# Kernel optimization log

Measured on AMD Instinct MI355X. Metric: run time of the kernel, lower is better.

The kernel has to match this reference:

```python
import jax, jax.numpy as jnp
import numpy as np

# Stack of L SSA transformer blocks (SMVDR conv_trans stages with sr_ratio=2)
L, B, N, C = 4, 64, 196, 768          # layers, batch(=16 samples x 4 views), tokens, dim
CN = 960                               # c_new = int(C * 1.25)
HID = 3072                             # mlp hidden = 4*C
NH = 12                                # heads
HD, HDK = C // NH, CN // NH            # v head dim 64, q/k head dim 80
SR, HW = 2, 14                         # spatial reduction ratio, sqrt(N)


def _ln(x, g, b, eps):
    m = jnp.mean(x, axis=-1, keepdims=True)
    v = jnp.var(x, axis=-1, keepdims=True)
    return (x - m) * jax.lax.rsqrt(v + eps) * g + b


def setup_inputs() -> dict:
    key = jax.random.key(0)
    ks = jax.random.split(key, 12)
    s = jnp.float32(0.02)

    def rn(k, shape):
        return jax.random.normal(k, shape, jnp.float32) * s

    return {
        "x": jax.random.normal(ks[0], (B, N, C), jnp.float32),
        "q_w": rn(ks[1], (L, C, CN)),                 # q projection (no bias)
        "dw_w": rn(ks[2], (L, C, 1, SR, SR)),         # depthwise reduction conv (OIHW, groups=C)
        "dw_b": jnp.zeros((L, C), jnp.float32),
        "pw_w": rn(ks[3], (L, C, CN)),                # 1x1 conv C -> c_new
        "pw_b": jnp.zeros((L, CN), jnp.float32),
        "lnr_g": jnp.ones((L, CN), jnp.float32),      # norm_act LayerNorm (eps 1e-5)
        "lnr_b": jnp.zeros((L, CN), jnp.float32),
        "k_w": rn(ks[4], (L, CN, CN)),
        "v_w": rn(ks[5], (L, CN, C)),
        "proj_w": rn(ks[6], (L, C, C)),
        "proj_b": jnp.zeros((L, C), jnp.float32),
        "ln1_g": jnp.ones((L, C), jnp.float32),
        "ln1_b": jnp.zeros((L, C), jnp.float32),
        "ln2_g": jnp.ones((L, C), jnp.float32),
        "ln2_b": jnp.zeros((L, C), jnp.float32),
        "fc1_w": rn(ks[7], (L, C, HID)),
        "fc1_b": jnp.zeros((L, HID), jnp.float32),
        "fc2_w": rn(ks[8], (L, HID, C)),
        "fc2_b": jnp.zeros((L, C), jnp.float32),
    }


def reference(x, q_w, dw_w, dw_b, pw_w, pw_b, lnr_g, lnr_b, k_w, v_w,
              proj_w, proj_b, ln1_g, ln1_b, ln2_g, ln2_b,
              fc1_w, fc1_b, fc2_w, fc2_b):
    scale = 1.0 / jnp.sqrt(jnp.float32(HD) * 1.25)   # (head_dim * c_ratio) ** -0.5
    for l in range(L):
        # --- SSA attention branch ---
        y = _ln(x, ln1_g[l], ln1_b[l], 1e-6)
        img = y.transpose(0, 2, 1).reshape(B, C, HW, HW)
        # strided depthwise conv reduction (kernel=stride=sr_ratio, groups=C)
        r = jax.lax.conv_general_dilated(
            img, dw_w[l], window_strides=(SR, SR), padding='VALID',
            feature_group_count=C,
            dimension_numbers=('NCHW', 'OIHW', 'NCHW'))
        r = r + dw_b[l][None, :, None, None]
        r = jnp.einsum('bchw,cd->bhwd', r, pw_w[l]) + pw_b[l]   # 1x1 conv -> (B,7,7,CN)
        r = r.reshape(B, -1, CN)                                 # (B, M=49, CN)
        r = jax.nn.gelu(_ln(r, lnr_g[l], lnr_b[l], 1e-5), approximate=False)
        q = (y @ q_w[l]).reshape(B, N, NH, HDK).transpose(0, 2, 1, 3)   # (B,H,N,80)
        k = (r @ k_w[l]).reshape(B, -1, NH, HDK).transpose(0, 2, 1, 3)  # (B,H,M,80)
        v = (r @ v_w[l]).reshape(B, -1, NH, HD).transpose(0, 2, 1, 3)   # (B,H,M,64)
        attn = jax.nn.softmax(jnp.einsum('bhnd,bhmd->bhnm', q, k) * scale, axis=-1)
        o = jnp.einsum('bhnm,bhmd->bnhd', attn, v).reshape(B, N, C)
        x = x + o @ proj_w[l] + proj_b[l]
        # --- MLP branch ---
        z = _ln(x, ln2_g[l], ln2_b[l], 1e-6)
        h = jax.nn.gelu(z @ fc1_w[l] + fc1_b[l], approximate=False)
        x = x + h @ fc2_w[l] + fc2_b[l]
    return x
```

## Files before the change

### kernel.cpp

```cpp
#include <hip/hip_runtime.h>
#include <hip/hip_bf16.h>
#include <math.h>

#define L_LAYERS 4
#define BSZ 64
#define NTOK 196
#define CDIM 768
#define CNDIM 960
#define HIDDIM 3072
#define NHEAD 12
#define HD 64
#define HDK 80
#define MRED 49
#define ROWS (BSZ*NTOK)
#define RROWS (BSZ*MRED)
#define KVN 1728

typedef __bf16 bf16x8 __attribute__((ext_vector_type(8)));
typedef float f32x4 __attribute__((ext_vector_type(4)));
typedef unsigned short u16x4 __attribute__((ext_vector_type(4)));

static __device__ inline float bf2f(unsigned short u) {
    unsigned int x = ((unsigned int)u) << 16;
    return __builtin_bit_cast(float, x);
}
static __device__ inline unsigned short f2bf(float f) {
    return __builtin_bit_cast(unsigned short, __float2bfloat16(f));
}
static __device__ inline unsigned int pack2bf(float lo, float hi) {
    return (unsigned int)f2bf(lo) | ((unsigned int)f2bf(hi) << 16);
}
static __device__ inline float gelu_f(float x) {
    float t = x * (1.5957691216f + 0.0713548162f * x * x);
    return x * __builtin_amdgcn_rcpf(1.0f + __expf(-t));
}

#define GLLDS16(gsrc, ldst)                                                        \
    __builtin_amdgcn_global_load_lds(                                              \
        (const __attribute__((address_space(1))) unsigned int*)(const void*)(gsrc),\
        (__attribute__((address_space(3))) unsigned int*)(void*)(ldst), 16, 0, 0)

__global__ void transpose_bf16_kernel(const float* __restrict__ src,
                                      unsigned short* __restrict__ dst,
                                      int K, int N, size_t srcLS, size_t dstLS) {
    __shared__ float tile[32][33];
    const float* s = src + (size_t)blockIdx.z * srcLS;
    unsigned short* d = dst + (size_t)blockIdx.z * dstLS;
    int k0 = blockIdx.y * 32, n0 = blockIdx.x * 32;
#pragma unroll
    for (int i = 0; i < 4; i++) {
        int k = k0 + threadIdx.y + i * 8, n = n0 + threadIdx.x;
        if (k < K && n < N) tile[threadIdx.y + i * 8][threadIdx.x] = s[(size_t)k * N + n];
    }
    __syncthreads();
#pragma unroll
    for (int i = 0; i < 4; i++) {
        int n = n0 + threadIdx.y + i * 8, k = k0 + threadIdx.x;
        if (n < N && k < K) d[(size_t)n * K + k] = f2bf(tile[threadIdx.x][threadIdx.y + i * 8]);
    }
}

__global__ void ln_kernel(const float* __restrict__ x, const float* __restrict__ g,
                          const float* __restrict__ b, unsigned short* __restrict__ y,
                          int M, int C, float eps, int do_gelu) {
    int row = blockIdx.x * 4 + (threadIdx.x >> 6);
    int lane = threadIdx.x & 63;
    if (row >= M) return;
    const float* xr = x + (size_t)row * C;
    float s = 0.f, ss = 0.f;
    for (int c = lane; c < C; c += 64) { float v = xr[c]; s += v; ss += v * v; }
#pragma unroll
    for (int off = 32; off; off >>= 1) { s += __shfl_down(s, off); ss += __shfl_down(ss, off); }
    s = __shfl(s, 0); ss = __shfl(ss, 0);
    float mean = s / (float)C;
    float var = ss / (float)C - mean * mean;
    float rstd = rsqrtf(var + eps);
    unsigned short* yr = y + (size_t)row * C;
    for (int c = lane; c < C; c += 64) {
        float v = (xr[c] - mean) * rstd * g[c] + b[c];
        if (do_gelu) v = gelu_f(v);
        yr[c] = f2bf(v);
    }
}

__global__ void dwconv_kernel(const unsigned short* __restrict__ y,
                              const float* __restrict__ w,
                              const float* __restrict__ bias,
                              unsigned short* __restrict__ r0) {
    int bm = blockIdx.x;
    int b = bm / MRED, m = bm % MRED;
    int i = m / 7, j = m % 7;
    int r00 = b * NTOK + (2 * i) * 14 + 2 * j;
    for (int c = threadIdx.x; c < CDIM; c += 256) {
        float acc = bias[c];
        acc += bf2f(y[(size_t)(r00)      * CDIM + c]) * w[c * 4 + 0];
        acc += bf2f(y[(size_t)(r00 + 1)  * CDIM + c]) * w[c * 4 + 1];
        acc += bf2f(y[(size_t)(r00 + 14) * CDIM + c]) * w[c * 4 + 2];
        acc += bf2f(y[(size_t)(r00 + 15) * CDIM + c]) * w[c * 4 + 3];
        r0[(size_t)bm * CDIM + c] = f2bf(acc);
    }
}

template <int MODE>
__global__ __launch_bounds__(512, 2) void gemm256_kernel(
    const unsigned short* __restrict__ A,
    const unsigned short* __restrict__ Bt,
    const float* __restrict__ bias,
    float* __restrict__ outF,
    unsigned short* __restrict__ outB,
    int M, int N, int K, int NR, int NC) {
    extern __shared__ __align__(16) char sb[];

    int id = blockIdx.x;
    int gsize = 8 * NC;
    int g = id / gsize;
    int local = id - g * gsize;
    int rbase = g * 8;
    int Gg = NR - rbase; if (Gg > 8) Gg = 8;
    int col = local / Gg;
    int row = rbase + (local - col * Gg);
    int m0 = row * 256, n0 = col * 256;

    int tid = threadIdx.x;
    int w = tid >> 6, lane = tid & 63, quad = lane >> 4, l16 = lane & 15;
    int wm = w >> 2, wn = w & 3;

    int sr = tid >> 2;
    int qs = ((tid & 3) - ((sr >> 1) & 3)) & 3;
    const unsigned short* aS0 = A  + (size_t)(m0 + sr) * K + qs * 8;
    const unsigned short* aS1 = A  + (size_t)(m0 + sr + 128) * K + qs * 8;
    const unsigned short* bS0 = Bt + (size_t)(n0 + sr) * K + qs * 8;
    const unsigned short* bS1 = Bt + (size_t)(n0 + sr + 128) * K + qs * 8;

    int sq16 = ((quad + (l16 >> 1)) & 3) * 16;
    int aOff = (wm * 128 + l16) * 64 + sq16;
    int bOff = 16384 + (wn * 64 + l16) * 64 + sq16;

    f32x4 zero4 = {0.f, 0.f, 0.f, 0.f};
    f32x4 acc[8][4];
#pragma unroll
    for (int mi = 0; mi < 8; mi++)
#pragma unroll
        for (int ni = 0; ni < 4; ni++) acc[mi][ni] = zero4;

    int NT = K >> 5;

#define STAGE256(slotptr, koff)                                  \
    do {                                                         \
        GLLDS16(aS0 + (koff), (slotptr) + w * 1024);             \
        GLLDS16(aS1 + (koff), (slotptr) + 8192  + w * 1024);     \
        GLLDS16(bS0 + (koff), (slotptr) + 16384 + w * 1024);     \
        GLLDS16(bS1 + (koff), (slotptr) + 24576 + w * 1024);     \
    } while (0)

    STAGE256(sb, 0);
    STAGE256(sb + 32768, 32);
    asm volatile("s_waitcnt vmcnt(4)" ::: "memory");
    __builtin_amdgcn_s_barrier();

    for (int t = 0; t < NT; ++t) {
        char* sc = sb + (size_t)(t & 3) * 32768;
        if (t + 2 < NT) {
            char* sp = sb + (size_t)((t + 2) & 3) * 32768;
            STAGE256(sp, (t + 2) * 32);
        }
        bf16x8 bfr[4], af[4];
#pragma unroll
        for (int ni = 0; ni < 4; ni++)
            bfr[ni] = *(const bf16x8*)(sc + bOff + ni * 1024);
#pragma unroll
        for (int mi = 0; mi < 4; mi++)
            af[mi] = *(const bf16x8*)(sc + aOff + mi * 1024);
        __builtin_amdgcn_s_setprio(1);
#pragma unroll
        for (int mi = 0; mi < 4; mi++)
#pragma unroll
            for (int ni = 0; ni < 4; ni++)
                acc[mi][ni] = __builtin_amdgcn_mfma_f32_16x16x32_bf16(
                    af[mi], bfr[ni], acc[mi][ni], 0, 0, 0);
        __builtin_amdgcn_s_setprio(0);
#pragma unroll
        for (int mi = 0; mi < 4; mi++)
            af[mi] = *(const bf16x8*)(sc + aOff + (mi + 4) * 1024);
        __builtin_amdgcn_s_setprio(1);
#pragma unroll
        for (int mi = 0; mi < 4; mi++)
#pragma unroll
            for (int ni = 0; ni < 4; ni++)
                acc[mi + 4][ni] = __builtin_amdgcn_mfma_f32_16x16x32_bf16(
                    af[mi], bfr[ni], acc[mi + 4][ni], 0, 0, 0);
        __builtin_amdgcn_s_setprio(0);
        if (t + 2 < NT) {
            asm volatile("s_waitcnt vmcnt(4)" ::: "memory");
        } else {
            asm volatile("s_waitcnt vmcnt(0)" ::: "memory");
        }
        __builtin_amdgcn_s_barrier();
    }
#undef STAGE256

    __syncthreads();
    float* eld = (float*)(sb + w * 16384);
    int colbase = n0 + wn * 64;
#pragma unroll
    for (int mi = 0; mi < 8; mi++) {
#pragma unroll
        for (int ni = 0; ni < 4; ni++)
#pragma unroll
            for (int rr = 0; rr < 4; rr++)
                eld[(quad * 4 + rr) * 64 + ni * 16 + l16] = acc[mi][ni][rr];
        int rowb = m0 + wm * 128 + mi * 16;
#pragma unroll
        for (int p = 0; p < 4; p++) {
            int r = p * 4 + quad;
            int c = l16 * 4;
            int gr = rowb + r, gc = colbase + c;
            if (gr < M && gc < N) {
                f32x4 v4 = *(f32x4*)(eld + r * 64 + c);
                if (MODE == 0) {
                    u16x4 h;
#pragma unroll
                    for (int e = 0; e < 4; e++) h[e] = f2bf(v4[e]);
                    *(u16x4*)(outB + (size_t)gr * N + gc) = h;
                } else {
                    f32x4 b4 = *(const f32x4*)(bias + gc);
                    if (MODE == 1) {
                        *(f32x4*)(outF + (size_t)gr * N + gc) = v4 + b4;
                    } else if (MODE == 2) {
                        f32x4 o4 = *(f32x4*)(outF + (size_t)gr * N + gc);
                        *(f32x4*)(outF + (size_t)gr * N + gc) = o4 + v4 + b4;
                    } else {
                        u16x4 h;
#pragma unroll
                        for (int e = 0; e < 4; e++) h[e] = f2bf(gelu_f(v4[e] + b4[e]));
                        *(u16x4*)(outB + (size_t)gr * N + gc) = h;
                    }
                }
            }
        }
    }
}

__global__ __launch_bounds__(512, 4) void attn_kernel(
    const unsigned short* __restrict__ qb,
    const unsigned short* __restrict__ kv,
    unsigned short* __restrict__ ob) {
    __shared__ __align__(16) unsigned short Ks[64 * 96];
    __shared__ __align__(16) unsigned short V2[64 * 136];
    __shared__ __align__(16) unsigned short Os[8 * 16 * 72];

    int bh = blockIdx.x;
    int b = bh / NHEAD, h = bh % NHEAD;
    int tid = threadIdx.x;

    for (int idx = tid; idx < 49 * 8; idx += 512) {
        int m = idx >> 3, c = idx & 7;
        ((unsigned int*)Ks)[m * 48 + 40 + c] = 0u;
    }
    for (int idx = tid; idx < 49 * 10; idx += 512) {
        int m = idx / 10, c = idx % 10;
        bf16x8 v = *(const bf16x8*)(kv + (size_t)(b * MRED + m) * KVN + h * HDK + c * 8);
        *(bf16x8*)(Ks + m * 96 + c * 8) = v;
    }
    for (int idx = tid; idx < 64 * 128; idx += 512) {
        int d = idx >> 7, c = idx & 127;
        int s = c >> 5, q = (c >> 3) & 3, j = c & 7;
        int kt = s * 32 + ((j >> 2) << 4) + q * 4 + (j & 3);
        unsigned short val = 0;
        if (kt < MRED) val = kv[(size_t)(b * MRED + kt) * KVN + 960 + h * HD + d];
        V2[d * 136 + c] = val;
    }
    __syncthreads();

    int wv = tid >> 6, lane = tid & 63, quad = lane >> 4, l16 = lane & 15;
    unsigned short* Ow = Os + wv * 16 * 72;
    const float scale = 0.11180339887498949f;
    f32x4 zero4 = {0.f, 0.f, 0.f, 0.f};

#pragma unroll
    for (int gi = 0; gi < 2; ++gi) {
        int qg = wv + gi * 8;
        if (qg >= 13) break;
        const unsigned short* qrow =
            qb + (size_t)(b * NTOK + qg * 16 + l16) * CNDIM + h * HDK + quad * 8;
        bf16x8 bq0 = *(const bf16x8*)(qrow);
        bf16x8 bq1 = *(const bf16x8*)(qrow + 32);
        bf16x8 bq2 = *(const bf16x8*)(qrow + 64);

        f32x4 sf[4];
#pragma unroll
        for (int kf = 0; kf < 4; kf++) sf[kf] = zero4;
#pragma unroll
        for (int kf = 0; kf < 4; kf++) {
            const unsigned short* kr = Ks + (kf * 16 + l16) * 96 + quad * 8;
            sf[kf] = __builtin_amdgcn_mfma_f32_16x16x32_bf16(
                *(const bf16x8*)(kr), bq0, sf[kf], 0, 0, 0);
            sf[kf] = __builtin_amdgcn_mfma_f32_16x16x32_bf16(
                *(const bf16x8*)(kr + 32), bq1, sf[kf], 0, 0, 0);
            sf[kf] = __builtin_amdgcn_mfma_f32_16x16x32_bf16(
                *(const bf16x8*)(kr + 64), bq2, sf[kf], 0, 0, 0);
        }

        float p[4][4];
        float mx = -1e30f;
#pragma unroll
        for (int kf = 0; kf < 4; kf++)
#pragma unroll
            for (int r = 0; r < 4; r++) {
                float v = sf[kf][r] * scale;
                if (kf == 3) {
                    v = (r == 0 && quad == 0) ? v : -1e30f;
                }
                p[kf][r] = v;
                mx = fmaxf(mx, v);
            }
        mx = fmaxf(mx, __shfl_xor(mx, 16));
        mx = fmaxf(mx, __shfl_xor(mx, 32));
        float sum = 0.f;
#pragma unroll
        for (int kf = 0; kf < 4; kf++)
#pragma unroll
            for (int r = 0; r < 4; r++) {
                float e = __expf(p[kf][r] - mx);
                p[kf][r] = e;
                sum += e;
            }
        sum += __shfl_xor(sum, 16);
        sum += __shfl_xor(sum, 32);
        float inv = 1.0f / sum;
#pragma unroll
        for (int kf = 0; kf < 4; kf++)
#pragma unroll
            for (int r = 0; r < 4; r++) p[kf][r] *= inv;

        unsigned int W[4][2];
#pragma unroll
        for (int kf = 0; kf < 4; kf++) {
            W[kf][0] = pack2bf(p[kf][0], p[kf][1]);
            W[kf][1] = pack2bf(p[kf][2], p[kf][3]);
        }

        f32x4 oacc[4];
#pragma unroll
        for (int df = 0; df < 4; df++) oacc[df] = zero4;
#pragma unroll
        for (int s = 0; s < 2; s++) {
            union { unsigned int u[4]; bf16x8 v; } bb;
            bb.u[0] = W[2 * s][0];
            bb.u[1] = W[2 * s][1];
            bb.u[2] = W[2 * s + 1][0];
            bb.u[3] = W[2 * s + 1][1];
#pragma unroll
            for (int df = 0; df < 4; df++) {
                const unsigned short* vr = V2 + (df * 16 + l16) * 136 + s * 32 + quad * 8;
                oacc[df] = __builtin_amdgcn_mfma_f32_16x16x32_bf16(
                    *(const bf16x8*)(vr), bb.v, oacc[df], 0, 0, 0);
            }
        }

#pragma unroll
        for (int df = 0; df < 4; df++) {
#pragma unroll
            for (int wp = 0; wp < 2; wp++) {
                unsigned int pk = pack2bf(oacc[df][2 * wp], oacc[df][2 * wp + 1]);
                *(unsigned int*)(Ow + l16 * 72 + df * 16 + quad * 4 + 2 * wp) = pk;
            }
        }
        int q = lane >> 2, cch = lane & 3;
        int grow = qg * 16 + q;
        if (grow < NTOK) {
            unsigned short* dst = ob + (size_t)(b * NTOK + grow) * CDIM + h * HD + cch * 8;
            bf16x8 v0 = *(const bf16x8*)(Ow + q * 72 + cch * 8);
            bf16x8 v1 = *(const bf16x8*)(Ow + q * 72 + cch * 8 + 32);
            *(bf16x8*)(dst) = v0;
            *(bf16x8*)(dst + 32) = v1;
        }
    }
}


extern "C" void kernel_launch(void* const* d_in, const int* in_sizes, int n_in,
                              void* d_out, int out_size, void* d_ws, size_t ws_size,
                              hipStream_t stream) {
    (void)in_sizes; (void)n_in; (void)out_size; (void)ws_size;
    const float* x_in   = (const float*)d_in[0];
    const float* q_w    = (const float*)d_in[1];
    const float* dw_w   = (const float*)d_in[2];
    const float* dw_b   = (const float*)d_in[3];
    const float* pw_w   = (const float*)d_in[4];
    const float* pw_b   = (const float*)d_in[5];
    const float* lnr_g  = (const float*)d_in[6];
    const float* lnr_b  = (const float*)d_in[7];
    const float* k_w    = (const float*)d_in[8];
    const float* v_w    = (const float*)d_in[9];
    const float* proj_w = (const float*)d_in[10];
    const float* proj_b = (const float*)d_in[11];
    const float* ln1_g  = (const float*)d_in[12];
    const float* ln1_b  = (const float*)d_in[13];
    const float* ln2_g  = (const float*)d_in[14];
    const float* ln2_b  = (const float*)d_in[15];
    const float* fc1_w  = (const float*)d_in[16];
    const float* fc1_b  = (const float*)d_in[17];
    const float* fc2_w  = (const float*)d_in[18];
    const float* fc2_b  = (const float*)d_in[19];
    float* xout = (float*)d_out;
    char* ws = (char*)d_ws;

    static bool attr_done = false;
    if (!attr_done) {
        hipFuncSetAttribute(reinterpret_cast<const void*>(&gemm256_kernel<0>),
                            hipFuncAttributeMaxDynamicSharedMemorySize, 131072);
        hipFuncSetAttribute(reinterpret_cast<const void*>(&gemm256_kernel<1>),
                            hipFuncAttributeMaxDynamicSharedMemorySize, 131072);
        hipFuncSetAttribute(reinterpret_cast<const void*>(&gemm256_kernel<2>),
                            hipFuncAttributeMaxDynamicSharedMemorySize, 131072);
        hipFuncSetAttribute(reinterpret_cast<const void*>(&gemm256_kernel<3>),
                            hipFuncAttributeMaxDynamicSharedMemorySize, 131072);
        attr_done = true;
    }

    const size_t PL = 8601600;
    const size_t offQ = 0, offPW = 786432, offKV = 1572864,
                 offPJ = 3293184, offF1 = 3883008, offF2 = 6242304;
    unsigned short* W = (unsigned short*)ws;
    char* act = ws + PL * 2 * L_LAYERS;
    unsigned short* y_bf = (unsigned short*)act;
    char* blk = act + (size_t)ROWS * CDIM * 2;
    unsigned short* q_bf  = (unsigned short*)(blk);
    unsigned short* r0_bf = (unsigned short*)(blk + 24084480);
    float*          pw_f  = (float*)        (blk + 29196288);
    unsigned short* r_bf  = (unsigned short*)(blk + 41238528);
    unsigned short* kv_bf = (unsigned short*)(blk + 47628288);
    unsigned short* o_bf  = (unsigned short*)(blk + 58466304);
    unsigned short* h_bf  = (unsigned short*)(blk);
    unsigned short* z_bf  = y_bf;

    hipMemcpyAsync(xout, x_in, (size_t)ROWS * CDIM * sizeof(float),
                   hipMemcpyDeviceToDevice, stream);

    dim3 tb(32, 8);
    transpose_bf16_kernel<<<dim3(CNDIM / 32, CDIM / 32, L_LAYERS), tb, 0, stream>>>(
        q_w, W + offQ, CDIM, CNDIM, (size_t)CDIM * CNDIM, PL);
    transpose_bf16_kernel<<<dim3(CNDIM / 32, CDIM / 32, L_LAYERS), tb, 0, stream>>>(
        pw_w, W + offPW, CDIM, CNDIM, (size_t)CDIM * CNDIM, PL);
    transpose_bf16_kernel<<<dim3(CNDIM / 32, CNDIM / 32, L_LAYERS), tb, 0, stream>>>(
        k_w, W + offKV, CNDIM, CNDIM, (size_t)CNDIM * CNDIM, PL);
    transpose_bf16_kernel<<<dim3(CDIM / 32, CNDIM / 32, L_LAYERS), tb, 0, stream>>>(
        v_w, W + offKV + (size_t)CNDIM * CNDIM, CNDIM, CDIM, (size_t)CNDIM * CDIM, PL);
    transpose_bf16_kernel<<<dim3(CDIM / 32, CDIM / 32, L_LAYERS), tb, 0, stream>>>(
        proj_w, W + offPJ, CDIM, CDIM, (size_t)CDIM * CDIM, PL);
    transpose_bf16_kernel<<<dim3(HIDDIM / 32, CDIM / 32, L_LAYERS), tb, 0, stream>>>(
        fc1_w, W + offF1, CDIM, HIDDIM, (size_t)CDIM * HIDDIM, PL);
    transpose_bf16_kernel<<<dim3(CDIM / 32, HIDDIM / 32, L_LAYERS), tb, 0, stream>>>(
        fc2_w, W + offF2, HIDDIM, CDIM, (size_t)HIDDIM * CDIM, PL);

    for (int l = 0; l < L_LAYERS; l++) {
        const unsigned short* wl = W + (size_t)l * PL;
        ln_kernel<<<ROWS / 4, 256, 0, stream>>>(xout, ln1_g + l * CDIM, ln1_b + l * CDIM,
                                                y_bf, ROWS, CDIM, 1e-6f, 0);
        gemm256_kernel<0><<<49 * 4, 512, 131072, stream>>>(
            y_bf, wl + offQ, nullptr, nullptr, q_bf, ROWS, CNDIM, CDIM, 49, 4);
        dwconv_kernel<<<RROWS, 256, 0, stream>>>(y_bf, dw_w + (size_t)l * CDIM * 4,
                                                 dw_b + l * CDIM, r0_bf);
        gemm256_kernel<1><<<13 * 4, 512, 131072, stream>>>(
            r0_bf, wl + offPW, pw_b + l * CNDIM, pw_f, nullptr, RROWS, CNDIM, CDIM, 13, 4);
        ln_kernel<<<RROWS / 4, 256, 0, stream>>>(pw_f, lnr_g + l * CNDIM, lnr_b + l * CNDIM,
                                                 r_bf, RROWS, CNDIM, 1e-5f, 1);
        gemm256_kernel<0><<<13 * 7, 512, 131072, stream>>>(
            r_bf, wl + offKV, nullptr, nullptr, kv_bf, RROWS, KVN, CNDIM, 13, 7);
        attn_kernel<<<BSZ * NHEAD, 512, 0, stream>>>(q_bf, kv_bf, o_bf);
        gemm256_kernel<2><<<49 * 3, 512, 131072, stream>>>(
            o_bf, wl + offPJ, proj_b + l * CDIM, xout, nullptr, ROWS, CDIM, CDIM, 49, 3);
        ln_kernel<<<ROWS / 4, 256, 0, stream>>>(xout, ln2_g + l * CDIM, ln2_b + l * CDIM,
                                                z_bf, ROWS, CDIM, 1e-6f, 0);
        gemm256_kernel<3><<<49 * 12, 512, 131072, stream>>>(
            z_bf, wl + offF1, fc1_b + l * HIDDIM, nullptr, h_bf, ROWS, HIDDIM, CDIM, 49, 12);
        gemm256_kernel<2><<<49 * 3, 512, 131072, stream>>>(
            h_bf, wl + offF2, fc2_b + l * CDIM, xout, nullptr, ROWS, CDIM, HIDDIM, 49, 3);
    }
}
```

Baseline: 1.813 ms.

## Replace 256x256 GEMM tiles with 128-row tiles and double-buffered LDS

The GEMM kernel drops from 256x256 tiles with a 4-slot, 2-ahead prefetch pipeline to 128xBN tiles (BN 256 or 128) with a 2-slot double buffer. Shared memory per block falls from 128KB to 32-48KB, and launch bounds ask for 4 blocks per CU. The goal is more blocks and better wave fill on the small M=3136 reduced-row GEMMs and the large GEMMs. In exchange, each tile reuses less data, the pipeline is shallower with a full vmcnt(0) wait every iteration, and global traffic for weights and activations rises.

```diff
diff --git a/kernel.cpp b/kernel.cpp
--- a/kernel.cpp
+++ b/kernel.cpp
@@ -101,14 +101,16 @@
     }
 }
 
-template <int MODE>
-__global__ __launch_bounds__(512, 2) void gemm256_kernel(
+template <int MODE, int BN>
+__global__ __launch_bounds__(512, 4) void gemm128_kernel(
     const unsigned short* __restrict__ A,
     const unsigned short* __restrict__ Bt,
     const float* __restrict__ bias,
     float* __restrict__ outF,
     unsigned short* __restrict__ outB,
     int M, int N, int K, int NR, int NC) {
+    constexpr int NFR = BN / 64;
+    constexpr int SLOT = 8192 + BN * 64;
     extern __shared__ __align__(16) char sb[];
 
     int id = blockIdx.x;
@@ -119,7 +121,7 @@
     int Gg = NR - rbase; if (Gg > 8) Gg = 8;
     int col = local / Gg;
     int row = rbase + (local - col * Gg);
-    int m0 = row * 256, n0 = col * 256;
+    int m0 = row * 128, n0 = col * BN;
 
     int tid = threadIdx.x;
     int w = tid >> 6, lane = tid & 63, quad = lane >> 4, l16 = lane & 15;
@@ -128,95 +130,78 @@
     int sr = tid >> 2;
     int qs = ((tid & 3) - ((sr >> 1) & 3)) & 3;
     const unsigned short* aS0 = A  + (size_t)(m0 + sr) * K + qs * 8;
-    const unsigned short* aS1 = A  + (size_t)(m0 + sr + 128) * K + qs * 8;
     const unsigned short* bS0 = Bt + (size_t)(n0 + sr) * K + qs * 8;
     const unsigned short* bS1 = Bt + (size_t)(n0 + sr + 128) * K + qs * 8;
 
     int sq16 = ((quad + (l16 >> 1)) & 3) * 16;
-    int aOff = (wm * 128 + l16) * 64 + sq16;
-    int bOff = 16384 + (wn * 64 + l16) * 64 + sq16;
+    int aOff = (wm * 64 + l16) * 64 + sq16;
+    int bOff = 8192 + (wn * (BN / 4) + l16) * 64 + sq16;
 
     f32x4 zero4 = {0.f, 0.f, 0.f, 0.f};
-    f32x4 acc[8][4];
-#pragma unroll
-    for (int mi = 0; mi < 8; mi++)
-#pragma unroll
-        for (int ni = 0; ni < 4; ni++) acc[mi][ni] = zero4;
+    f32x4 acc[4][NFR];
+#pragma unroll
+    for (int mi = 0; mi < 4; mi++)
+#pragma unroll
+        for (int ni = 0; ni < NFR; ni++) acc[mi][ni] = zero4;
 
     int NT = K >> 5;
 
-#define STAGE256(slotptr, koff)                                  \
-    do {                                                         \
-        GLLDS16(aS0 + (koff), (slotptr) + w * 1024);             \
-        GLLDS16(aS1 + (koff), (slotptr) + 8192  + w * 1024);     \
-        GLLDS16(bS0 + (koff), (slotptr) + 16384 + w * 1024);     \
-        GLLDS16(bS1 + (koff), (slotptr) + 24576 + w * 1024);     \
-    } while (0)
-
-    STAGE256(sb, 0);
-    STAGE256(sb + 32768, 32);
-    asm volatile("s_waitcnt vmcnt(4)" ::: "memory");
+    {
+        GLLDS16(aS0, sb + w * 1024);
+        GLLDS16(bS0, sb + 8192 + w * 1024);
+        if constexpr (BN == 256) GLLDS16(bS1, sb + 16384 + w * 1024);
+    }
+    asm volatile("s_waitcnt vmcnt(0)" ::: "memory");
     __builtin_amdgcn_s_barrier();
 
     for (int t = 0; t < NT; ++t) {
-        char* sc = sb + (size_t)(t & 3) * 32768;
-        if (t + 2 < NT) {
-            char* sp = sb + (size_t)((t + 2) & 3) * 32768;
-            STAGE256(sp, (t + 2) * 32);
-        }
-        bf16x8 bfr[4], af[4];
-#pragma unroll
-        for (int ni = 0; ni < 4; ni++)
-            bfr[ni] = *(const bf16x8*)(sc + bOff + ni * 1024);
+        char* sc = sb + (size_t)(t & 1) * SLOT;
+        if (t + 1 < NT) {
+            char* sp = sb + (size_t)((t + 1) & 1) * SLOT;
+            int koff = (t + 1) * 32;
+            GLLDS16(aS0 + koff, sp + w * 1024);
+            GLLDS16(bS0 + koff, sp + 8192 + w * 1024);
+            if constexpr (BN == 256) GLLDS16(bS1 + koff, sp + 16384 + w * 1024);
+        }
+        bf16x8 af[4], bfr[NFR];
 #pragma unroll
         for (int mi = 0; mi < 4; mi++)
             af[mi] = *(const bf16x8*)(sc + aOff + mi * 1024);
+#pragma unroll
+        for (int ni = 0; ni < NFR; ni++)
+            bfr[ni] = *(const bf16x8*)(sc + bOff + ni * 1024);
         __builtin_amdgcn_s_setprio(1);
 #pragma unroll
         for (int mi = 0; mi < 4; mi++)
 #pragma unroll
-            for (int ni = 0; ni < 4; ni++)
+            for (int ni = 0; ni < NFR; ni++)
                 acc[mi][ni] = __builtin_amdgcn_mfma_f32_16x16x32_bf16(
                     af[mi], bfr[ni], acc[mi][ni], 0, 0, 0);
         __builtin_amdgcn_s_setprio(0);
-#pragma unroll
-        for (int mi = 0; mi < 4; mi++)
-            af[mi] = *(const bf16x8*)(sc + aOff + (mi + 4) * 1024);
-        __builtin_amdgcn_s_setprio(1);
-#pragma unroll
-        for (int mi = 0; mi < 4; mi++)
-#pragma unroll
-            for (int ni = 0; ni < 4; ni++)
-                acc[mi + 4][ni] = __builtin_amdgcn_mfma_f32_16x16x32_bf16(
-                    af[mi], bfr[ni], acc[mi + 4][ni], 0, 0, 0);
-        __builtin_amdgcn_s_setprio(0);
-        if (t + 2 < NT) {
-            asm volatile("s_waitcnt vmcnt(4)" ::: "memory");
-        } else {
-            asm volatile("s_waitcnt vmcnt(0)" ::: "memory");
-        }
+        asm volatile("s_waitcnt vmcnt(0)" ::: "memory");
         __builtin_amdgcn_s_barrier();
     }
-#undef STAGE256
 
     __syncthreads();
-    float* eld = (float*)(sb + w * 16384);
-    int colbase = n0 + wn * 64;
-#pragma unroll
-    for (int mi = 0; mi < 8; mi++) {
-#pragma unroll
-        for (int ni = 0; ni < 4; ni++)
+    float* eld = (float*)(sb + w * (BN == 256 ? 4096 : 2048));
+    int colbase = n0 + wn * (BN / 4);
+#pragma unroll
+    for (int mi = 0; mi < 4; mi++) {
+#pragma unroll
+        for (int ni = 0; ni < NFR; ni++)
 #pragma unroll
             for (int rr = 0; rr < 4; rr++)
-                eld[(quad * 4 + rr) * 64 + ni * 16 + l16] = acc[mi][ni][rr];
-        int rowb = m0 + wm * 128 + mi * 16;
-#pragma unroll
-        for (int p = 0; p < 4; p++) {
-            int r = p * 4 + quad;
-            int c = l16 * 4;
+                eld[(quad * 4 + rr) * (BN / 4) + ni * 16 + l16] = acc[mi][ni][rr];
+        int rowb = m0 + wm * 64 + mi * 16;
+        constexpr int NP = (BN == 256) ? 4 : 2;
+#pragma unroll
+        for (int p = 0; p < NP; p++) {
+            int r, c;
+            if constexpr (BN == 256) { r = p * 4 + quad;        c = l16 * 4; }
+            else                     { r = p * 8 + (lane >> 3); c = (lane & 7) * 4; }
             int gr = rowb + r, gc = colbase + c;
             if (gr < M && gc < N) {
-                f32x4 v4 = *(f32x4*)(eld + r * 64 + c);
+                f32x4 v4 = *(f32x4*)(eld + r * (BN / 4) + c);
                 if (MODE == 0) {
                     u16x4 h;
 #pragma unroll
@@ -406,19 +391,6 @@
     float* xout = (float*)d_out;
     char* ws = (char*)d_ws;
 
-    static bool attr_done = false;
-    if (!attr_done) {
-        hipFuncSetAttribute(reinterpret_cast<const void*>(&gemm256_kernel<0>),
-                            hipFuncAttributeMaxDynamicSharedMemorySize, 131072);
-        hipFuncSetAttribute(reinterpret_cast<const void*>(&gemm256_kernel<1>),
-                            hipFuncAttributeMaxDynamicSharedMemorySize, 131072);
-        hipFuncSetAttribute(reinterpret_cast<const void*>(&gemm256_kernel<2>),
-                            hipFuncAttributeMaxDynamicSharedMemorySize, 131072);
-        hipFuncSetAttribute(reinterpret_cast<const void*>(&gemm256_kernel<3>),
-                            hipFuncAttributeMaxDynamicSharedMemorySize, 131072);
-        attr_done = true;
-    }
-
     const size_t PL = 8601600;
     const size_t offQ = 0, offPW = 786432, offKV = 1572864,
                  offPJ = 3293184, offF1 = 3883008, offF2 = 6242304;
@@ -458,24 +430,24 @@
         const unsigned short* wl = W + (size_t)l * PL;
         ln_kernel<<<ROWS / 4, 256, 0, stream>>>(xout, ln1_g + l * CDIM, ln1_b + l * CDIM,
                                                 y_bf, ROWS, CDIM, 1e-6f, 0);
-        gemm256_kernel<0><<<49 * 4, 512, 131072, stream>>>(
-            y_bf, wl + offQ, nullptr, nullptr, q_bf, ROWS, CNDIM, CDIM, 49, 4);
+        gemm128_kernel<0, 256><<<98 * 4, 512, 49152, stream>>>(
+            y_bf, wl + offQ, nullptr, nullptr, q_bf, ROWS, CNDIM, CDIM, 98, 4);
         dwconv_kernel<<<RROWS, 256, 0, stream>>>(y_bf, dw_w + (size_t)l * CDIM * 4,
                                                  dw_b + l * CDIM, r0_bf);
-        gemm256_kernel<1><<<13 * 4, 512, 131072, stream>>>(
-            r0_bf, wl + offPW, pw_b + l * CNDIM, pw_f, nullptr, RROWS, CNDIM, CDIM, 13, 4);
+        gemm128_kernel<1, 128><<<25 * 8, 512, 32768, stream>>>(
+            r0_bf, wl + offPW, pw_b + l * CNDIM, pw_f, nullptr, RROWS, CNDIM, CDIM, 25, 8);
         ln_kernel<<<RROWS / 4, 256, 0, stream>>>(pw_f, lnr_g + l * CNDIM, lnr_b + l * CNDIM,
                                                  r_bf, RROWS, CNDIM, 1e-5f, 1);
-        gemm256_kernel<0><<<13 * 7, 512, 131072, stream>>>(
-            r_bf, wl + offKV, nullptr, nullptr, kv_bf, RROWS, KVN, CNDIM, 13, 7);
+        gemm128_kernel<0, 128><<<25 * 14, 512, 32768, stream>>>(
+            r_bf, wl + offKV, nullptr, nullptr, kv_bf, RROWS, KVN, CNDIM, 25, 14);
         attn_kernel<<<BSZ * NHEAD, 512, 0, stream>>>(q_bf, kv_bf, o_bf);
-        gemm256_kernel<2><<<49 * 3, 512, 131072, stream>>>(
-            o_bf, wl + offPJ, proj_b + l * CDIM, xout, nullptr, ROWS, CDIM, CDIM, 49, 3);
+        gemm128_kernel<2, 256><<<98 * 3, 512, 49152, stream>>>(
+            o_bf, wl + offPJ, proj_b + l * CDIM, xout, nullptr, ROWS, CDIM, CDIM, 98, 3);
         ln_kernel<<<ROWS / 4, 256, 0, stream>>>(xout, ln2_g + l * CDIM, ln2_b + l * CDIM,
                                                 z_bf, ROWS, CDIM, 1e-6f, 0);
-        gemm256_kernel<3><<<49 * 12, 512, 131072, stream>>>(
-            z_bf, wl + offF1, fc1_b + l * HIDDIM, nullptr, h_bf, ROWS, HIDDIM, CDIM, 49, 12);
-        gemm256_kernel<2><<<49 * 3, 512, 131072, stream>>>(
-            h_bf, wl + offF2, fc2_b + l * CDIM, xout, nullptr, ROWS, CDIM, HIDDIM, 49, 3);
-    }
-}
+        gemm128_kernel<3, 256><<<98 * 12, 512, 49152, stream>>>(
+            z_bf, wl + offF1, fc1_b + l * HIDDIM, nullptr, h_bf, ROWS, HIDDIM, CDIM, 98, 12);
+        gemm128_kernel<2, 256><<<98 * 3, 512, 49152, stream>>>(
+            h_bf, wl + offF2, fc2_b + l * CDIM, xout, nullptr, ROWS, CDIM, HIDDIM, 98, 3);
+    }
+}
```

Result: faster. 1.597 ms (-11.9%).
